# Kernel optimization log

Hardware: AMD Instinct MI355X
Metric: run time of the kernel (lower is better)

## Reference

```python
import jax, jax.numpy as jnp
import numpy as np

PATCH = 16  # patch_size

def _patchify(images, p=PATCH):
    # images: [B, H, W] -> patches: [B, N, p*p] in raster order
    B, H, W = images.shape
    x = images.reshape(B, H // p, p, W // p, p)
    x = x.transpose(0, 1, 3, 2, 4)  # [B, H/p, W/p, p, p]
    return x.reshape(B, (H // p) * (W // p), p * p)

def setup_inputs() -> dict:
    key = jax.random.key(0)
    k1, k2 = jax.random.split(key)
    images = jax.random.normal(k1, (64, 256, 256), dtype=jnp.float32)
    vocab = jax.random.normal(k2, (4096, 256), dtype=jnp.float32)  # [V, patch^2]
    return {"images": images, "vocab": vocab}

def reference(images, vocab):
    # forward_patches: patchify (raster ordering -> identity permutation)
    patches = _patchify(images)  # [B, N, D]
    # forward_tokens: torch.cdist + argmin. argmin of Euclidean distance
    # equals argmin of squared distance; expand ||x-v||^2 to avoid the
    # explicit [B, N, V, D] difference tensor.
    v2 = jnp.sum(vocab * vocab, axis=-1)                      # [V]
    xv = jnp.einsum('bnd,vd->bnv', patches, vocab)            # [B, N, V]
    x2 = jnp.sum(patches * patches, axis=-1, keepdims=True)   # [B, N, 1]
    d2 = x2 - 2.0 * xv + v2                                   # [B, N, V]
    tokens = jnp.argmin(d2, axis=-1)                          # [B, N] int
    return patches, tokens
```

## Files before the change

kernel.cpp:

```cpp
#include <hip/hip_runtime.h>
#include <math.h>

#define PS      16
#define D       256
#define V       4096
#define M       16384
#define NSPLIT  16
#define PAIR_CAP 1048576
#define QMARGIN 130

typedef _Float16 half8 __attribute__((ext_vector_type(8)));
typedef _Float16 half4 __attribute__((ext_vector_type(4)));
typedef float    f32x4 __attribute__((ext_vector_type(4)));

__device__ __forceinline__ void gload_lds16(const void* g, void* l) {
  __builtin_amdgcn_global_load_lds(
      (const __attribute__((address_space(1))) unsigned int*)g,
      (__attribute__((address_space(3))) unsigned int*)l, 16, 0, 0);
}

__global__ __launch_bounds__(256) void prep_kernel(
    const float* __restrict__ img, const float* __restrict__ vocab,
    float* __restrict__ outp, _Float16* __restrict__ Ah,
    _Float16* __restrict__ Vh, float* __restrict__ v2,
    int* __restrict__ paircount) {
  if (blockIdx.x < 4096) {
    if (blockIdx.x == 0 && threadIdx.x == 0) *paircount = 0;
    const int t  = blockIdx.x * 256 + threadIdx.x;
    const int o4 = t << 2;
    const int b   = o4 >> 16;
    const int rem = o4 & 65535;
    const int n   = rem >> 8;
    const int d   = rem & 255;
    const int py = n >> 4, px = n & 15, i = d >> 4, j = d & 15;
    const float4 v = *(const float4*)(img + (b << 16) + ((py * PS + i) << 8) + px * PS + j);
    *(float4*)(outp + o4) = v;
    half4 h = { (_Float16)v.x, (_Float16)v.y, (_Float16)v.z, (_Float16)v.w };
    *(half4*)(Ah + o4) = h;
  } else {
    const int gtid = (blockIdx.x - 4096) * 256 + threadIdx.x;
    const int row  = gtid >> 6;
    const int lane = gtid & 63;
    const float4 v = *(const float4*)(vocab + (size_t)row * D + (lane << 2));
    half4 h = { (_Float16)v.x, (_Float16)v.y, (_Float16)v.z, (_Float16)v.w };
    *(half4*)(Vh + (size_t)row * D + (lane << 2)) = h;
    float s = v.x * v.x + v.y * v.y + v.z * v.z + v.w * v.w;
    #pragma unroll
    for (int off = 32; off > 0; off >>= 1) s += __shfl_down(s, off);
    if (lane == 0) v2[row] = s;
  }
}

__global__ __launch_bounds__(256, 3) void gemm_score_kernel(
    const _Float16* __restrict__ Ah,
    const _Float16* __restrict__ Vh,
    const float* __restrict__ v2,
    unsigned* __restrict__ pk1, unsigned* __restrict__ pk2) {
  __shared__ __align__(16) _Float16 Af[8 * 64 * 32];
  __shared__ unsigned eK1[64][4];
  __shared__ unsigned eK2[64][4];

  const int tid  = threadIdx.x;
  const int lane = tid & 63;
  const int wid  = tid >> 6;
  const int row0 = blockIdx.x * 64;
  const int sp   = blockIdx.y;
  const int col0 = sp * 256 + wid * 64;

  {
    const int srow = lane >> 2;
    const int sg   = ((lane & 3) ^ ((srow >> 1) & 3)) << 3;
    const _Float16* Ag = Ah + (size_t)(row0 + wid * 16 + srow) * D + sg;
    _Float16* Al = Af + wid * 16 * 32;
    #pragma unroll
    for (int kt = 0; kt < 8; ++kt)
      gload_lds16(Ag + kt * 32, Al + kt * 64 * 32);
  }
  __syncthreads();

  const int cl = lane & 15;
  const int q  = lane >> 4;
  const int fg = (q ^ ((cl >> 1) & 3)) << 3;
  const _Float16* Ab = Af + cl * 32 + fg;

  const _Float16* Bp = Vh + (size_t)(col0 + cl) * D + q * 8;

  f32x4 acc[4][4];
  #pragma unroll
  for (int i = 0; i < 4; ++i)
    #pragma unroll
    for (int j = 0; j < 4; ++j) acc[i][j] = (f32x4){0.f, 0.f, 0.f, 0.f};

  #pragma unroll 1
  for (int kt = 0; kt < 8; ++kt) {
    half8 b[4];
    #pragma unroll
    for (int j = 0; j < 4; ++j)
      b[j] = *(const half8*)(Bp + (size_t)j * 16 * D + kt * 32);
    half8 af[4];
    #pragma unroll
    for (int i = 0; i < 4; ++i)
      af[i] = *(const half8*)(Ab + kt * 2048 + i * 512);
    #pragma unroll
    for (int i = 0; i < 4; ++i)
      #pragma unroll
      for (int j = 0; j < 4; ++j)
        acc[i][j] = __builtin_amdgcn_mfma_f32_16x16x32_f16(af[i], b[j], acc[i][j], 0, 0, 0);
  }

  float Cj[4];
  #pragma unroll
  for (int j = 0; j < 4; ++j) Cj[j] = fmaf(v2[col0 + j * 16 + cl], 512.0f, 524288.0f);
  unsigned kk1[16], kk2[16];
  #pragma unroll
  for (int i = 0; i < 4; ++i)
    #pragma unroll
    for (int r = 0; r < 4; ++r) {
      const int p = i * 4 + r;
      unsigned K1 = 0xFFFFFFFFu, K2 = 0xFFFFFFFFu;
      #pragma unroll
      for (int j = 0; j < 4; ++j) {
        const unsigned key =
            ((unsigned)fmaf(-1024.0f, acc[i][j][r], Cj[j]) << 12) |
            (unsigned)(col0 + j * 16 + cl);
        K2 = min(K2, max(K1, key));
        K1 = min(K1, key);
      }
      kk1[p] = K1; kk2[p] = K2;
    }
  #pragma unroll
  for (int p = 0; p < 16; ++p) {
    unsigned k1 = kk1[p], k2 = kk2[p];
    #pragma unroll
    for (int mask = 1; mask <= 8; mask <<= 1) {
      const unsigned o1 = (unsigned)__shfl_xor((int)k1, mask);
      const unsigned o2 = (unsigned)__shfl_xor((int)k2, mask);
      k2 = min(min(k2, o2), max(k1, o1));
      k1 = min(k1, o1);
    }
    kk1[p] = k1; kk2[p] = k2;
  }
  if (cl == 0) {
    #pragma unroll
    for (int p = 0; p < 16; ++p) {
      const int rl = (p >> 2) * 16 + q * 4 + (p & 3);
      eK1[rl][wid] = kk1[p]; eK2[rl][wid] = kk2[p];
    }
  }
  __syncthreads();
  if (tid < 64) {
    unsigned K1 = 0xFFFFFFFFu, K2 = 0xFFFFFFFFu;
    #pragma unroll
    for (int w = 0; w < 4; ++w) {
      const unsigned b1 = eK1[tid][w], b2 = eK2[tid][w];
      K2 = min(min(K2, b2), max(K1, b1));
      K1 = min(K1, b1);
    }
    pk1[(size_t)sp * M + row0 + tid] = K1;
    pk2[(size_t)sp * M + row0 + tid] = K2;
  }
}

__global__ __launch_bounds__(256) void reduce_gather_kernel(
    const unsigned* __restrict__ pk1, const unsigned* __restrict__ pk2,
    float* __restrict__ tok, unsigned long long* __restrict__ minkey,
    unsigned* __restrict__ pairs, int* __restrict__ paircount) {
  const int m = blockIdx.x * 256 + threadIdx.x;
  unsigned K1 = 0xFFFFFFFFu, K2 = 0xFFFFFFFFu;
  for (int s = 0; s < NSPLIT; ++s) {
    const unsigned b1 = pk1[(size_t)s * M + m];
    const unsigned b2 = pk2[(size_t)s * M + m];
    K2 = min(min(K2, b2), max(K1, b1));
    K1 = min(K1, b1);
  }
  tok[m] = (float)(K1 & 4095u);
  minkey[m] = 0xFFFFFFFFFFFFFFFFull;
  if ((int)(K2 >> 12) - (int)(K1 >> 12) <= QMARGIN) {
    const int th = (int)(K1 >> 12) + QMARGIN;
    int cnt = 0;
    for (int s = 0; s < NSPLIT; ++s) {
      const unsigned b1 = pk1[(size_t)s * M + m];
      const unsigned b2 = pk2[(size_t)s * M + m];
      cnt += ((int)(b2 >> 12) <= th) ? 256
           : (((int)(b1 >> 12) <= th) ? 1 : 0);
    }
    int base = atomicAdd(paircount, cnt);
    if (base + cnt <= PAIR_CAP) {
      const unsigned mh = (unsigned)m << 12;
      for (int s = 0; s < NSPLIT; ++s) {
        const unsigned b1 = pk1[(size_t)s * M + m];
        const unsigned b2 = pk2[(size_t)s * M + m];
        if ((int)(b2 >> 12) <= th) {
          for (int r = 0; r < 256; ++r) pairs[base + r] = mh | (unsigned)(s * 256 + r);
          base += 256;
        } else if ((int)(b1 >> 12) <= th) {
          pairs[base++] = mh | (b1 & 4095u);
        }
      }
    }
  }
}

__global__ __launch_bounds__(256) void refine_score(
    const float* __restrict__ patches, const float* __restrict__ vocab,
    const unsigned* __restrict__ pairs, const int* __restrict__ paircount,
    unsigned long long* __restrict__ minkey) {
  const int lane = threadIdx.x & 63;
  const int gw = (blockIdx.x * 256 + threadIdx.x) >> 6;
  const int nw = (gridDim.x * 256) >> 6;
  int np = *paircount;
  if (np > PAIR_CAP) np = PAIR_CAP;
  for (int i = gw; i < np; i += nw) {
    const unsigned pr = pairs[i];
    const int m = pr >> 12, row = pr & 4095;
    const float4 pv = *(const float4*)(patches + (size_t)m * D + (lane << 2));
    const float4 vv = *(const float4*)(vocab + (size_t)row * D + (lane << 2));
    double acc = 0.0, df;
    df = (double)pv.x - (double)vv.x; acc = fma(df, df, acc);
    df = (double)pv.y - (double)vv.y; acc = fma(df, df, acc);
    df = (double)pv.z - (double)vv.z; acc = fma(df, df, acc);
    df = (double)pv.w - (double)vv.w; acc = fma(df, df, acc);
    #pragma unroll
    for (int off = 32; off > 0; off >>= 1) acc += __shfl_down(acc, off);
    if (lane == 0) {
      const unsigned long long key =
          ((unsigned long long)__double_as_longlong(acc) & ~0xFFFull) | (unsigned)row;
      atomicMin(&minkey[m], key);
    }
  }
}

__global__ __launch_bounds__(256) void refine_final(
    const unsigned* __restrict__ pairs, const int* __restrict__ paircount,
    const unsigned long long* __restrict__ minkey, float* __restrict__ tok) {
  int np = *paircount;
  if (np > PAIR_CAP) np = PAIR_CAP;
  for (int i = blockIdx.x * 256 + threadIdx.x; i < np; i += gridDim.x * 256) {
    const int m = pairs[i] >> 12;
    tok[m] = (float)(unsigned)(minkey[m] & 4095ull);
  }
}

extern "C" void kernel_launch(void* const* d_in, const int* in_sizes, int n_in,
                              void* d_out, int out_size, void* d_ws, size_t ws_size,
                              hipStream_t stream) {
  const float* images = (const float*)d_in[0];
  const float* vocab  = (const float*)d_in[1];
  float* out     = (float*)d_out;
  float* patches = out;
  float* tokens  = out + (size_t)M * D;

  char* ws = (char*)d_ws;
  _Float16* Ah       = (_Float16*)(ws);
  _Float16* Vh       = (_Float16*)(ws + 8388608);
  float*    v2       = (float*)   (ws + 10485760);
  unsigned* pk1      = (unsigned*)(ws + 10502144);
  unsigned* pk2      = (unsigned*)(ws + 11550720);
  unsigned long long* minkey = (unsigned long long*)(ws + 12599296);
  int*      paircount= (int*)     (ws + 12730368);
  unsigned* pairs    = (unsigned*)(ws + 12730432);

  prep_kernel<<<4096 + 1024, 256, 0, stream>>>(images, vocab, patches, Ah,
                                               Vh, v2, paircount);
  gemm_score_kernel<<<dim3(M / 64, NSPLIT), 256, 0, stream>>>(Ah, Vh, v2, pk1, pk2);
  reduce_gather_kernel<<<M / 256, 256, 0, stream>>>(pk1, pk2, tokens, minkey,
                                                    pairs, paircount);
  refine_score<<<512, 256, 0, stream>>>(patches, vocab, pairs, paircount, minkey);
  refine_final<<<64, 256, 0, stream>>>(pairs, paircount, minkey, tokens);
}
```

Measured before the change: 172.8 us.

## Write per-wave top-2 keys directly and software-prefetch MFMA operands

The GEMM kernel no longer merges the four waves' top-2 keys through shared memory behind a block barrier. Each wave now writes its own top-2 partial for its 64-column group, so there are 64 splits instead of 16, and the fallback pair expansion shrinks from 256 to 64 candidates per tie. The inner k-loop double-buffers the B and A fragment loads so the next step's loads are issued before the current MFMAs. In exchange, the partial buffers are four times larger and the reduce kernel reads four times more partials per row.

```diff
diff --git a/kernel.cpp b/kernel.cpp
--- a/kernel.cpp
+++ b/kernel.cpp
@@ -5,7 +5,7 @@
 #define D       256
 #define V       4096
 #define M       16384
-#define NSPLIT  16
+#define NSPLIT  64
 #define PAIR_CAP 1048576
 #define QMARGIN 130
 
@@ -57,8 +57,6 @@
     const float* __restrict__ v2,
     unsigned* __restrict__ pk1, unsigned* __restrict__ pk2) {
   __shared__ __align__(16) _Float16 Af[8 * 64 * 32];
-  __shared__ unsigned eK1[64][4];
-  __shared__ unsigned eK2[64][4];
 
   const int tid  = threadIdx.x;
   const int lane = tid & 63;
@@ -66,6 +64,7 @@
   const int row0 = blockIdx.x * 64;
   const int sp   = blockIdx.y;
   const int col0 = sp * 256 + wid * 64;
+  const int grp  = sp * 4 + wid;
 
   {
     const int srow = lane >> 2;
@@ -82,7 +81,6 @@
   const int q  = lane >> 4;
   const int fg = (q ^ ((cl >> 1) & 3)) << 3;
   const _Float16* Ab = Af + cl * 32 + fg;
-
   const _Float16* Bp = Vh + (size_t)(col0 + cl) * D + q * 8;
 
   f32x4 acc[4][4];
@@ -90,17 +88,28 @@
   for (int i = 0; i < 4; ++i)
     #pragma unroll
     for (int j = 0; j < 4; ++j) acc[i][j] = (f32x4){0.f, 0.f, 0.f, 0.f};
+
+  half8 bn[4], afn[4];
+  #pragma unroll
+  for (int j = 0; j < 4; ++j) bn[j] = *(const half8*)(Bp + (size_t)j * 16 * D);
+  #pragma unroll
+  for (int i = 0; i < 4; ++i) afn[i] = *(const half8*)(Ab + i * 512);
 
   #pragma unroll 1
   for (int kt = 0; kt < 8; ++kt) {
-    half8 b[4];
-    #pragma unroll
-    for (int j = 0; j < 4; ++j)
-      b[j] = *(const half8*)(Bp + (size_t)j * 16 * D + kt * 32);
-    half8 af[4];
-    #pragma unroll
-    for (int i = 0; i < 4; ++i)
-      af[i] = *(const half8*)(Ab + kt * 2048 + i * 512);
+    half8 b[4], af[4];
+    #pragma unroll
+    for (int j = 0; j < 4; ++j) b[j] = bn[j];
+    #pragma unroll
+    for (int i = 0; i < 4; ++i) af[i] = afn[i];
+    if (kt < 7) {
+      #pragma unroll
+      for (int j = 0; j < 4; ++j)
+        bn[j] = *(const half8*)(Bp + (size_t)j * 16 * D + (kt + 1) * 32);
+      #pragma unroll
+      for (int i = 0; i < 4; ++i)
+        afn[i] = *(const half8*)(Ab + (kt + 1) * 2048 + i * 512);
+    }
     #pragma unroll
     for (int i = 0; i < 4; ++i)
       #pragma unroll
@@ -144,20 +153,9 @@
     #pragma unroll
     for (int p = 0; p < 16; ++p) {
       const int rl = (p >> 2) * 16 + q * 4 + (p & 3);
-      eK1[rl][wid] = kk1[p]; eK2[rl][wid] = kk2[p];
-    }
-  }
-  __syncthreads();
-  if (tid < 64) {
-    unsigned K1 = 0xFFFFFFFFu, K2 = 0xFFFFFFFFu;
-    #pragma unroll
-    for (int w = 0; w < 4; ++w) {
-      const unsigned b1 = eK1[tid][w], b2 = eK2[tid][w];
-      K2 = min(min(K2, b2), max(K1, b1));
-      K1 = min(K1, b1);
-    }
-    pk1[(size_t)sp * M + row0 + tid] = K1;
-    pk2[(size_t)sp * M + row0 + tid] = K2;
+      pk1[(size_t)grp * M + row0 + rl] = kk1[p];
+      pk2[(size_t)grp * M + row0 + rl] = kk2[p];
+    }
   }
 }
 
@@ -181,7 +179,7 @@
     for (int s = 0; s < NSPLIT; ++s) {
       const unsigned b1 = pk1[(size_t)s * M + m];
       const unsigned b2 = pk2[(size_t)s * M + m];
-      cnt += ((int)(b2 >> 12) <= th) ? 256
+      cnt += ((int)(b2 >> 12) <= th) ? 64
            : (((int)(b1 >> 12) <= th) ? 1 : 0);
     }
     int base = atomicAdd(paircount, cnt);
@@ -191,8 +189,8 @@
         const unsigned b1 = pk1[(size_t)s * M + m];
         const unsigned b2 = pk2[(size_t)s * M + m];
         if ((int)(b2 >> 12) <= th) {
-          for (int r = 0; r < 256; ++r) pairs[base + r] = mh | (unsigned)(s * 256 + r);
-          base += 256;
+          for (int r = 0; r < 64; ++r) pairs[base + r] = mh | (unsigned)(s * 64 + r);
+          base += 64;
         } else if ((int)(b1 >> 12) <= th) {
           pairs[base++] = mh | (b1 & 4095u);
         }
@@ -255,14 +253,14 @@
   _Float16* Vh       = (_Float16*)(ws + 8388608);
   float*    v2       = (float*)   (ws + 10485760);
   unsigned* pk1      = (unsigned*)(ws + 10502144);
-  unsigned* pk2      = (unsigned*)(ws + 11550720);
-  unsigned long long* minkey = (unsigned long long*)(ws + 12599296);
-  int*      paircount= (int*)     (ws + 12730368);
-  unsigned* pairs    = (unsigned*)(ws + 12730432);
+  unsigned* pk2      = (unsigned*)(ws + 14696448);
+  unsigned long long* minkey = (unsigned long long*)(ws + 18890752);
+  int*      paircount= (int*)     (ws + 19021824);
+  unsigned* pairs    = (unsigned*)(ws + 19021888);
 
   prep_kernel<<<4096 + 1024, 256, 0, stream>>>(images, vocab, patches, Ah,
                                                Vh, v2, paircount);
-  gemm_score_kernel<<<dim3(M / 64, NSPLIT), 256, 0, stream>>>(Ah, Vh, v2, pk1, pk2);
+  gemm_score_kernel<<<dim3(M / 64, V / 256), 256, 0, stream>>>(Ah, Vh, v2, pk1, pk2);
   reduce_gather_kernel<<<M / 256, 256, 0, stream>>>(pk1, pk2, tokens, minkey,
                                                     pairs, paircount);
   refine_score<<<512, 256, 0, stream>>>(patches, vocab, pairs, paircount, minkey);
```

New measurement: 185.8 us. 1.07x slower.
